# Kernel tuning notes

Measured on AMD Instinct MI355X. Metric: run time of the kernel, lower is better.

The kernel has to match this reference:

```python
import jax, jax.numpy as jnp
import numpy as np

B, S, D = 2, 2048, 4096
H, KVH, HD = 32, 8, 128
ROPE_THETA = 10000.0

def setup_inputs() -> dict:
    key = jax.random.key(0)
    ks = jax.random.split(key, 5)
    x = jax.random.normal(ks[0], (B, S, D), jnp.float32)
    wq = jax.random.normal(ks[1], (D, H * HD), jnp.float32) * 0.02
    wk = jax.random.normal(ks[2], (D, KVH * HD), jnp.float32) * 0.02
    wv = jax.random.normal(ks[3], (D, KVH * HD), jnp.float32) * 0.02
    wo = jax.random.normal(ks[4], (H * HD, D), jnp.float32) * 0.02
    pos = jnp.arange(S, dtype=jnp.float32)
    inv_freq = 1.0 / (ROPE_THETA ** (jnp.arange(0, HD, 2, dtype=jnp.float32) / HD))
    freqs = pos[:, None] * inv_freq[None, :]  # [S, HD//2]
    return {"x": x, "cos": jnp.cos(freqs), "sin": jnp.sin(freqs),
            "wq": wq, "wk": wk, "wv": wv, "wo": wo, "start_pos": 0}

def _apply_rope(t, cos, sin):
    # t: [B, S, nh, HD]; rotate consecutive pairs (llama complex rotation)
    t = t.reshape(*t.shape[:-1], HD // 2, 2)
    t1, t2 = t[..., 0], t[..., 1]
    c = cos[None, :, None, :]
    s = sin[None, :, None, :]
    out = jnp.stack([t1 * c - t2 * s, t1 * s + t2 * c], axis=-1)
    return out.reshape(*out.shape[:-2], HD)

def reference(x, cos, sin, wq, wk, wv, wo, start_pos):
    b, s, _ = x.shape
    scale = 1.0 / np.sqrt(HD)
    xq = (x @ wq).reshape(b, s, H, HD)
    xk = (x @ wk).reshape(b, s, KVH, HD)
    xv = (x @ wv).reshape(b, s, KVH, HD)
    xq = _apply_rope(xq, cos, sin)
    xk = _apply_rope(xk, cos, sin)
    # start_pos == 0 prefill: cache write then read of [:s] is identity
    n_rep = H // KVH
    keys = jnp.repeat(xk, n_rep, axis=2)    # [b, s, H, HD]
    values = jnp.repeat(xv, n_rep, axis=2)
    q = xq.transpose(0, 2, 1, 3)            # [b, H, s, HD]
    k = keys.transpose(0, 2, 1, 3)
    v = values.transpose(0, 2, 1, 3)
    scores = jnp.einsum('bhqd,bhkd->bhqk', q, k) * scale
    mask = jnp.triu(jnp.full((s, s), -jnp.inf, dtype=scores.dtype), k=1)
    scores = scores + mask[None, None]
    attn = jax.nn.softmax(scores.astype(jnp.float32), axis=-1).astype(q.dtype)
    out = jnp.einsum('bhqk,bhkd->bhqd', attn, v)
    out = out.transpose(0, 2, 1, 3).reshape(b, s, H * HD)
    return out @ wo
```

## Files before the change

kernel.cpp:

```cpp
#include <hip/hip_runtime.h>

typedef __bf16 bf16_t;
typedef __bf16 bf16x8 __attribute__((ext_vector_type(8)));
typedef __bf16 bf16x4 __attribute__((ext_vector_type(4)));
typedef float  f32x4  __attribute__((ext_vector_type(4)));
typedef float  f32x16 __attribute__((ext_vector_type(16)));

#define NB   2
#define NS   2048
#define ND   4096
#define NH   32
#define NKVH 8
#define NHD  128

#define BAR()     asm volatile("s_barrier" ::: "memory")
#define LGKM0()   asm volatile("s_waitcnt lgkmcnt(0)" ::: "memory")
#define VMCNT10() asm volatile("s_waitcnt vmcnt(10)" ::: "memory")
#define VMCNT8()  asm volatile("s_waitcnt vmcnt(8)" ::: "memory")
#define VMCNT6()  asm volatile("s_waitcnt vmcnt(6)" ::: "memory")
#define VMCNT0()  asm volatile("s_waitcnt vmcnt(0)" ::: "memory")

__device__ __forceinline__ void gl_lds16(const bf16_t* g, bf16_t* l) {
  __builtin_amdgcn_global_load_lds(
      (const __attribute__((address_space(1))) void*)g,
      (__attribute__((address_space(3))) void*)l, 16, 0, 0);
}

__global__ void convert_f32_bf16(const float* __restrict__ in, bf16_t* __restrict__ out, int n4) {
  int i = blockIdx.x * 256 + threadIdx.x;
  if (i < n4) {
    f32x4 v = *(const f32x4*)&in[(size_t)i * 4];
    bf16x4 o;
    #pragma unroll
    for (int j = 0; j < 4; ++j) o[j] = (bf16_t)v[j];
    *(bf16x4*)&out[(size_t)i * 4] = o;
  }
}

__global__ void transpose_convert(const float* __restrict__ in, bf16_t* __restrict__ out, int Nin) {
  __shared__ float t[32][33];
  int tx = threadIdx.x & 31, ty = threadIdx.x >> 5;
  int n0 = blockIdx.x * 32, k0 = blockIdx.y * 32;
  #pragma unroll
  for (int i = 0; i < 4; ++i)
    t[ty + i * 8][tx] = in[(size_t)(k0 + ty + i * 8) * Nin + n0 + tx];
  __syncthreads();
  #pragma unroll
  for (int i = 0; i < 4; ++i)
    out[(size_t)(n0 + ty + i * 8) * 4096 + k0 + tx] = (bf16_t)t[tx][ty + i * 8];
}

__global__ __launch_bounds__(256, 2) void gemm192(const bf16_t* __restrict__ A,
                                                  const bf16_t* __restrict__ Bt,
                                                  bf16_t* __restrict__ C, int M, int N, int K) {
  __shared__ __align__(16) bf16_t As[2][128 * 64];
  __shared__ __align__(16) bf16_t Bs[2][192 * 64];
  const int tid = threadIdx.x, lane = tid & 63, wid = tid >> 6;
  const int l15 = lane & 15, l4 = lane >> 4;
  const int wm = wid >> 1, wn = wid & 1;

  const int gx = gridDim.x;
  const int nwg = gx * gridDim.y;
  const int id = blockIdx.y * gx + blockIdx.x;
  const int wg = (id & 7) * (nwg >> 3) + (id >> 3);
  const int bx = wg % gx, by = wg / gx;
  const int row0 = bx * 128, col0 = by * 192;

  const bf16_t* Ab = A + (size_t)row0 * K;
  const bf16_t* Bb = Bt + (size_t)col0 * K;

  auto stA = [&](int t, int buf) {
    #pragma unroll
    for (int i = 0; i < 4; ++i) {
      int phys = i * 4096 + tid * 16;
      int logi = phys ^ (((phys >> 8) & 7) << 4);
      gl_lds16(Ab + (size_t)(logi >> 7) * K + t * 64 + ((logi & 127) >> 1),
               &As[buf][phys >> 1]);
    }
  };
  auto stB = [&](int t, int buf) {
    #pragma unroll
    for (int i = 0; i < 6; ++i) {
      int phys = i * 4096 + tid * 16;
      int logi = phys ^ (((phys >> 8) & 7) << 4);
      gl_lds16(Bb + (size_t)(logi >> 7) * K + t * 64 + ((logi & 127) >> 1),
               &Bs[buf][phys >> 1]);
    }
  };

  f32x4 acc[4][6];
  #pragma unroll
  for (int m = 0; m < 4; ++m)
    #pragma unroll
    for (int n = 0; n < 6; ++n)
      #pragma unroll
      for (int j = 0; j < 4; ++j) acc[m][n][j] = 0.f;

  const int nt = K >> 6;
  stA(0, 0); stB(0, 0);
  stA(1, 1); stB(1, 1);
  VMCNT10();
  BAR();

  auto ardA = [&](int buf, int mf, int kh) -> bf16x8 {
    int lb = (wm * 64 + mf * 16 + l15) * 128 + kh * 64 + l4 * 16;
    return *(const bf16x8*)&As[buf][(lb ^ (((lb >> 8) & 7) << 4)) >> 1];
  };
  auto brdB = [&](int buf, int kh, int nf) -> bf16x8 {
    int lb = (wn * 96 + nf * 16 + l15) * 128 + kh * 64 + l4 * 16;
    return *(const bf16x8*)&Bs[buf][(lb ^ (((lb >> 8) & 7) << 4)) >> 1];
  };

  #pragma unroll 2
  for (int t = 0; t < nt; ++t) {
    const int cur = t & 1;
    bf16x8 a[4][2], b0[6], b1[6];

    #pragma unroll
    for (int mf = 0; mf < 4; ++mf)
      #pragma unroll
      for (int kh = 0; kh < 2; ++kh) a[mf][kh] = ardA(cur, mf, kh);
    #pragma unroll
    for (int nf = 0; nf < 6; ++nf) b0[nf] = brdB(cur, 0, nf);
    BAR();
    LGKM0();
    __builtin_amdgcn_s_setprio(1);
    #pragma unroll
    for (int mf = 0; mf < 4; ++mf)
      #pragma unroll
      for (int nf = 0; nf < 6; ++nf)
        acc[mf][nf] = __builtin_amdgcn_mfma_f32_16x16x32_bf16(a[mf][0], b0[nf], acc[mf][nf], 0, 0, 0);
    __builtin_amdgcn_s_setprio(0);
    BAR();

    #pragma unroll
    for (int nf = 0; nf < 6; ++nf) b1[nf] = brdB(cur, 1, nf);
    if (t + 2 < nt) { stA(t + 2, cur); stB(t + 2, cur); }
    BAR();
    LGKM0();
    __builtin_amdgcn_s_setprio(1);
    #pragma unroll
    for (int mf = 0; mf < 4; ++mf)
      #pragma unroll
      for (int nf = 0; nf < 6; ++nf)
        acc[mf][nf] = __builtin_amdgcn_mfma_f32_16x16x32_bf16(a[mf][1], b1[nf], acc[mf][nf], 0, 0, 0);
    __builtin_amdgcn_s_setprio(0);
    if (t + 2 < nt) { VMCNT10(); } else { VMCNT0(); }
    BAR();
  }

  #pragma unroll
  for (int mf = 0; mf < 4; ++mf)
    #pragma unroll
    for (int nf = 0; nf < 6; ++nf)
      #pragma unroll
      for (int r = 0; r < 4; ++r) {
        size_t row = (size_t)row0 + wm * 64 + mf * 16 + l4 * 4 + r;
        size_t col = (size_t)col0 + wn * 96 + nf * 16 + l15;
        C[row * N + col] = (bf16_t)acc[mf][nf][r];
      }
}

__global__ __launch_bounds__(512, 2) void gemm256j(const bf16_t* __restrict__ A,
                                                   const bf16_t* __restrict__ Bt,
                                                   float* __restrict__ C, int M, int N, int K) {
  __shared__ __align__(16) bf16_t As[2][2][128 * 64];
  __shared__ __align__(16) bf16_t Bs[2][256 * 64];
  const int tid = threadIdx.x, lane = tid & 63, wid = tid >> 6;
  const int l15 = lane & 15, l4 = lane >> 4;
  const int wm = wid >> 2, wn = wid & 3;

  const int gx = gridDim.x;
  const int nwg = gx * gridDim.y;
  const int id = blockIdx.y * gx + blockIdx.x;
  const int wg = (id & 7) * (nwg >> 3) + (id >> 3);
  const int bx = wg % gx, by = wg / gx;
  const int row0 = bx * 256, col0 = by * 256;

  const bf16_t* Ab = A + (size_t)row0 * K;
  const bf16_t* Bb = Bt + (size_t)col0 * K;

  auto stA = [&](int t, int h, int buf) {
    #pragma unroll
    for (int i = 0; i < 2; ++i) {
      int phys = i * 8192 + tid * 16;
      int logi = phys ^ (((phys >> 8) & 7) << 4);
      gl_lds16(Ab + (size_t)(h * 128 + (logi >> 7)) * K + t * 64 + ((logi & 127) >> 1),
               &As[buf][h][phys >> 1]);
    }
  };
  auto stB = [&](int t, int buf) {
    #pragma unroll
    for (int i = 0; i < 4; ++i) {
      int phys = i * 8192 + tid * 16;
      int logi = phys ^ (((phys >> 8) & 7) << 4);
      gl_lds16(Bb + (size_t)(logi >> 7) * K + t * 64 + ((logi & 127) >> 1),
               &Bs[buf][phys >> 1]);
    }
  };

  f32x4 acc[8][4];
  #pragma unroll
  for (int m = 0; m < 8; ++m)
    #pragma unroll
    for (int n = 0; n < 4; ++n)
      #pragma unroll
      for (int j = 0; j < 4; ++j) acc[m][n][j] = 0.f;

  const int nt = K >> 6;
  stA(0, 0, 0); stA(0, 1, 0); stB(0, 0);
  stA(1, 0, 1); stB(1, 1);
  VMCNT6();
  BAR();

  auto ardA = [&](int buf, int mh, int kh, int mf) -> bf16x8 {
    int lb = (mh * 64 + mf * 16 + l15) * 128 + kh * 64 + l4 * 16;
    return *(const bf16x8*)&As[buf][wm][(lb ^ (((lb >> 8) & 7) << 4)) >> 1];
  };
  auto brdB = [&](int buf, int kh, int nf) -> bf16x8 {
    int lb = (wn * 64 + nf * 16 + l15) * 128 + kh * 64 + l4 * 16;
    return *(const bf16x8*)&Bs[buf][(lb ^ (((lb >> 8) & 7) << 4)) >> 1];
  };

  #pragma unroll 2
  for (int t = 0; t < nt; ++t) {
    const int cur = t & 1, nxt = cur ^ 1;
    bf16x8 a00[4], a01[4], a10[4], a11[4], b0[4], b1[4];

    #pragma unroll
    for (int mf = 0; mf < 4; ++mf) a00[mf] = ardA(cur, 0, 0, mf);
    #pragma unroll
    for (int nf = 0; nf < 4; ++nf) b0[nf] = brdB(cur, 0, nf);
    #pragma unroll
    for (int mf = 0; mf < 4; ++mf) a01[mf] = ardA(cur, 0, 1, mf);
    #pragma unroll
    for (int nf = 0; nf < 4; ++nf) b1[nf] = brdB(cur, 1, nf);
    if (t + 1 < nt) stA(t + 1, 1, nxt);
    BAR();
    LGKM0();
    __builtin_amdgcn_s_setprio(1);
    #pragma unroll
    for (int mf = 0; mf < 4; ++mf)
      #pragma unroll
      for (int nf = 0; nf < 4; ++nf)
        acc[mf][nf] = __builtin_amdgcn_mfma_f32_16x16x32_bf16(a00[mf], b0[nf], acc[mf][nf], 0, 0, 0);
    #pragma unroll
    for (int mf = 0; mf < 4; ++mf)
      #pragma unroll
      for (int nf = 0; nf < 4; ++nf)
        acc[mf][nf] = __builtin_amdgcn_mfma_f32_16x16x32_bf16(a01[mf], b1[nf], acc[mf][nf], 0, 0, 0);
    __builtin_amdgcn_s_setprio(0);
    BAR();

    #pragma unroll
    for (int mf = 0; mf < 4; ++mf) a10[mf] = ardA(cur, 1, 0, mf);
    #pragma unroll
    for (int mf = 0; mf < 4; ++mf) a11[mf] = ardA(cur, 1, 1, mf);
    if (t + 2 < nt) { stA(t + 2, 0, cur); stB(t + 2, cur); }
    BAR();
    LGKM0();
    __builtin_amdgcn_s_setprio(1);
    #pragma unroll
    for (int mf = 0; mf < 4; ++mf)
      #pragma unroll
      for (int nf = 0; nf < 4; ++nf)
        acc[4 + mf][nf] = __builtin_amdgcn_mfma_f32_16x16x32_bf16(a10[mf], b0[nf], acc[4 + mf][nf], 0, 0, 0);
    #pragma unroll
    for (int mf = 0; mf < 4; ++mf)
      #pragma unroll
      for (int nf = 0; nf < 4; ++nf)
        acc[4 + mf][nf] = __builtin_amdgcn_mfma_f32_16x16x32_bf16(a11[mf], b1[nf], acc[4 + mf][nf], 0, 0, 0);
    __builtin_amdgcn_s_setprio(0);
    if (t + 2 < nt) { VMCNT6(); } else { VMCNT0(); }
    BAR();
  }

  #pragma unroll
  for (int mh = 0; mh < 2; ++mh)
    #pragma unroll
    for (int mf = 0; mf < 4; ++mf)
      #pragma unroll
      for (int nf = 0; nf < 4; ++nf)
        #pragma unroll
        for (int r = 0; r < 4; ++r) {
          size_t row = (size_t)row0 + wm * 128 + mh * 64 + mf * 16 + l4 * 4 + r;
          size_t col = (size_t)col0 + wn * 64 + nf * 16 + l15;
          C[row * N + col] = acc[mh * 4 + mf][nf][r];
        }
}

__global__ void rope_qk(const bf16_t* __restrict__ qkv, const float* __restrict__ cosT,
                        const float* __restrict__ sinT, bf16_t* __restrict__ Q,
                        bf16_t* __restrict__ Kout) {
  int it = blockIdx.x * 256 + threadIdx.x;
  int chunk = it & 15;
  int hs = (it >> 4) % 40;
  int m = (it >> 4) / 40;
  int b = m >> 11, srow = m & 2047;

  bf16x8 v = *(const bf16x8*)&qkv[(size_t)m * 6144 + hs * 128 + chunk * 8];
  f32x4 c4 = *(const f32x4*)&cosT[(size_t)srow * 64 + chunk * 4];
  f32x4 s4 = *(const f32x4*)&sinT[(size_t)srow * 64 + chunk * 4];
  bf16x8 o;
  #pragma unroll
  for (int j = 0; j < 4; ++j) {
    float t1 = (float)v[2 * j], t2 = (float)v[2 * j + 1];
    o[2 * j]     = (bf16_t)(t1 * c4[j] - t2 * s4[j]);
    o[2 * j + 1] = (bf16_t)(t1 * s4[j] + t2 * c4[j]);
  }
  bf16_t* dst;
  if (hs < 32) dst = Q + (((size_t)(b * 32 + hs)) * 2048 + srow) * 128 + chunk * 8;
  else         dst = Kout + (((size_t)(b * 8 + (hs - 32))) * 2048 + srow) * 128 + chunk * 8;
  *(bf16x8*)dst = o;
}

__global__ void transpose_v(const bf16_t* __restrict__ qkv, bf16_t* __restrict__ Vt) {
  __shared__ bf16_t t[32][33];
  int tx = threadIdx.x & 31, ty = threadIdx.x >> 5;
  int s0 = blockIdx.x * 32, d0 = blockIdx.y * 32, g = blockIdx.z;
  int b = g >> 3, kv = g & 7;
  const bf16_t* src = qkv + (size_t)(b * 2048) * 6144 + 5120 + kv * 128;
  #pragma unroll
  for (int i = 0; i < 4; ++i)
    t[ty + i * 8][tx] = src[(size_t)(s0 + ty + i * 8) * 6144 + d0 + tx];
  __syncthreads();
  bf16_t* dst = Vt + (size_t)g * 128 * 2048;
  #pragma unroll
  for (int i = 0; i < 4; ++i)
    dst[(size_t)(d0 + ty + i * 8) * 2048 + s0 + tx] = t[tx][ty + i * 8];
}

__global__ __launch_bounds__(256, 2) void attn_kernel(const bf16_t* __restrict__ Q,
                                                      const bf16_t* __restrict__ Kc,
                                                      const bf16_t* __restrict__ Vt,
                                                      bf16_t* __restrict__ Oout) {
  __shared__ __align__(16) bf16_t Ks[2][64 * 128];
  __shared__ __align__(16) bf16_t Vs[2][128 * 64];

  const int tid = threadIdx.x, wid = tid >> 6, lane = tid & 63;
  const int l31 = lane & 31, hi = lane >> 5;
  const int bh = blockIdx.y;
  const int b = bh >> 5, h = bh & 31, kv = h >> 2;
  const int pr = blockIdx.x;

  const bf16_t* Qp = Q + ((size_t)bh * 2048) * 128;
  const bf16_t* Kp = Kc + ((size_t)(b * 8 + kv) * 2048) * 128;
  const bf16_t* Vp = Vt + ((size_t)(b * 8 + kv) * 128) * 2048;

  const float kscale = 0.08838834764831845f * 1.44269504088896f;

  auto stage = [&](int kt, int buf) {
    const int k0 = kt * 64;
    #pragma unroll
    for (int i = 0; i < 4; ++i) {
      int phys = i * 4096 + tid * 16;
      int logi = phys ^ (((phys >> 8) & 15) << 4);
      gl_lds16(Kp + (size_t)(k0 + (phys >> 8)) * 128 + ((logi & 255) >> 1), &Ks[buf][phys >> 1]);
    }
    #pragma unroll
    for (int i = 0; i < 4; ++i) {
      int phys = i * 4096 + tid * 16;
      int logi = phys ^ (((phys >> 7) & 7) << 4);
      gl_lds16(Vp + (size_t)(phys >> 7) * 2048 + k0 + ((logi & 127) >> 1), &Vs[buf][phys >> 1]);
    }
  };

  for (int half = 0; half < 2; ++half) {
    const int qt = half ? pr : 15 - pr;
    const int q0b = qt * 128;
    const int q0w = q0b + wid * 32;
    const int qg = q0w + l31;
    const int nkt = (qt + 1) * 2;

    bf16x8 qf[8];
    #pragma unroll
    for (int c = 0; c < 8; ++c) {
      bf16x8 t = *(const bf16x8*)&Qp[(size_t)qg * 128 + c * 16 + hi * 8];
      #pragma unroll
      for (int j = 0; j < 8; ++j) t[j] = (bf16_t)((float)t[j] * kscale);
      qf[c] = t;
    }

    f32x16 oa[4];
    #pragma unroll
    for (int nc = 0; nc < 4; ++nc)
      #pragma unroll
      for (int r = 0; r < 16; ++r) oa[nc][r] = 0.f;
    float m_old = -1e30f, lrow = 0.f;

    stage(0, 0);

    for (int kt = 0; kt < nkt; ++kt) {
      const int k0 = kt * 64, cur = kt & 1;
      if (kt + 1 < nkt) { stage(kt + 1, cur ^ 1); VMCNT8(); } else { VMCNT0(); }
      BAR();

      if (k0 <= q0w + 31) {
        f32x16 s0, s1;
        #pragma unroll
        for (int r = 0; r < 16; ++r) { s0[r] = 0.f; s1[r] = 0.f; }
        __builtin_amdgcn_s_setprio(1);
        #pragma unroll
        for (int c = 0; c < 8; ++c) {
          int lb0 = l31 * 256 + c * 32 + hi * 16;
          int pb0 = lb0 ^ (((lb0 >> 8) & 15) << 4);
          bf16x8 kf0 = *(const bf16x8*)&Ks[cur][pb0 >> 1];
          s0 = __builtin_amdgcn_mfma_f32_32x32x16_bf16(kf0, qf[c], s0, 0, 0, 0);
          int lb1 = (32 + l31) * 256 + c * 32 + hi * 16;
          int pb1 = lb1 ^ (((lb1 >> 8) & 15) << 4);
          bf16x8 kf1 = *(const bf16x8*)&Ks[cur][pb1 >> 1];
          s1 = __builtin_amdgcn_mfma_f32_32x32x16_bf16(kf1, qf[c], s1, 0, 0, 0);
        }
        __builtin_amdgcn_s_setprio(0);

        if (k0 + 63 > q0w) {
          #pragma unroll
          for (int r = 0; r < 16; ++r) {
            int key0 = k0 + ((r & 3) + 8 * (r >> 2)) + 4 * hi;
            if (key0 > qg) s0[r] = -1e30f;
            if (key0 + 32 > qg) s1[r] = -1e30f;
          }
        }

        float m8[8];
        #pragma unroll
        for (int j = 0; j < 8; ++j)
          m8[j] = fmaxf(fmaxf(s0[j], s0[j + 8]), fmaxf(s1[j], s1[j + 8]));
        float ma = fmaxf(fmaxf(m8[0], m8[4]), fmaxf(m8[1], m8[5]));
        float mb = fmaxf(fmaxf(m8[2], m8[6]), fmaxf(m8[3], m8[7]));
        float mh = fmaxf(ma, mb);
        float mfull = fmaxf(mh, __shfl_xor(mh, 32));

        float mn;
        bool defer = (mfull - m_old <= 8.0f);
        if (__all((int)defer)) {
          mn = m_old;
        } else {
          mn = fmaxf(m_old, mfull);
          float sc = exp2f(m_old - mn);
          #pragma unroll
          for (int r = 0; r < 16; ++r) {
            int qi = (r & 3) + 8 * (r >> 2) + 4 * hi;
            float scv = __int_as_float(__builtin_amdgcn_ds_bpermute(qi << 2, __float_as_int(sc)));
            oa[0][r] *= scv; oa[1][r] *= scv; oa[2][r] *= scv; oa[3][r] *= scv;
          }
          lrow *= sc;
          m_old = mn;
        }

        #pragma unroll
        for (int r = 0; r < 16; ++r) {
          s0[r] = exp2f(s0[r] - mn);
          s1[r] = exp2f(s1[r] - mn);
        }
        float rsA = 0.f, rsB = 0.f, rsC = 0.f, rsD = 0.f;
        #pragma unroll
        for (int r = 0; r < 16; r += 4) {
          rsA += s0[r];     rsB += s0[r + 1]; rsC += s0[r + 2]; rsD += s0[r + 3];
          rsA += s1[r];     rsB += s1[r + 1]; rsC += s1[r + 2]; rsD += s1[r + 3];
        }
        float rs = (rsA + rsB) + (rsC + rsD);
        rs += __shfl_xor(rs, 32);
        lrow = lrow + rs;

        #pragma unroll
        for (int ks = 0; ks < 4; ++ks) {
          const int qi0 = (ks & 1) * 8;
          union { bf16_t hh[4]; int ii[2]; } ku, su;
          #pragma unroll
          for (int j = 0; j < 4; ++j) {
            float lo, hv;
            if (ks >> 1) { lo = s1[qi0 + j]; hv = s1[qi0 + 4 + j]; }
            else         { lo = s0[qi0 + j]; hv = s0[qi0 + 4 + j]; }
            ku.hh[j] = (bf16_t)(hi ? hv : lo);
            su.hh[j] = (bf16_t)(hi ? lo : hv);
          }
          int r0 = __shfl_xor(su.ii[0], 32), r1 = __shfl_xor(su.ii[1], 32);
          union { int ii[4]; bf16x8 v; } fa;
          fa.ii[0] = hi ? r0 : ku.ii[0];
          fa.ii[1] = hi ? r1 : ku.ii[1];
          fa.ii[2] = hi ? ku.ii[0] : r0;
          fa.ii[3] = hi ? ku.ii[1] : r1;
          __builtin_amdgcn_s_setprio(1);
          #pragma unroll
          for (int nc = 0; nc < 4; ++nc) {
            int lb = (nc * 32 + l31) * 128 + ks * 32 + hi * 16;
            int pb = lb ^ (((lb >> 7) & 7) << 4);
            bf16x8 vf = *(const bf16x8*)&Vs[cur][pb >> 1];
            oa[nc] = __builtin_amdgcn_mfma_f32_32x32x16_bf16(fa.v, vf, oa[nc], 0, 0, 0);
          }
          __builtin_amdgcn_s_setprio(0);
        }
      }
      BAR();
    }

    float inv = 1.0f / lrow;
    bf16_t* Op = Oout + ((size_t)(b * 2048 + q0w)) * 4096 + (size_t)h * 128;
    #pragma unroll
    for (int r = 0; r < 16; ++r) {
      int qi = (r & 3) + 8 * (r >> 2) + 4 * hi;
      float iv = __int_as_float(__builtin_amdgcn_ds_bpermute(qi << 2, __float_as_int(inv)));
      #pragma unroll
      for (int nc = 0; nc < 4; ++nc)
        Op[(size_t)qi * 4096 + nc * 32 + l31] = (bf16_t)(oa[nc][r] * iv);
    }
  }
}

extern "C" void kernel_launch(void* const* d_in, const int* in_sizes, int n_in,
                              void* d_out, int out_size, void* d_ws, size_t ws_size,
                              hipStream_t stream) {
  const float* x    = (const float*)d_in[0];
  const float* cosT = (const float*)d_in[1];
  const float* sinT = (const float*)d_in[2];
  const float* wq   = (const float*)d_in[3];
  const float* wk   = (const float*)d_in[4];
  const float* wv   = (const float*)d_in[5];
  const float* wo   = (const float*)d_in[6];
  float* out = (float*)d_out;
  char* ws = (char*)d_ws;

  bf16_t* wqkvT = (bf16_t*)(ws + 0);
  bf16_t* woT   = wqkvT;
  bf16_t* xb    = (bf16_t*)(ws + 50331648);
  bf16_t* Qb    = xb;
  bf16_t* qkv   = (bf16_t*)(ws + 83886080);
  bf16_t* attn_out = qkv;
  bf16_t* Kb    = (bf16_t*)(ws + 134217728);
  bf16_t* Vt    = (bf16_t*)(ws + 142606336);

  convert_f32_bf16<<<16384, 256, 0, stream>>>(x, xb, 4194304);
  transpose_convert<<<dim3(128, 128), 256, 0, stream>>>(wq, wqkvT, 4096);
  transpose_convert<<<dim3(32, 128), 256, 0, stream>>>(wk, wqkvT + (size_t)4096 * 4096, 1024);
  transpose_convert<<<dim3(32, 128), 256, 0, stream>>>(wv, wqkvT + (size_t)5120 * 4096, 1024);

  gemm192<<<dim3(32, 32), 256, 0, stream>>>(xb, wqkvT, qkv, 4096, 6144, 4096);

  transpose_convert<<<dim3(128, 128), 256, 0, stream>>>(wo, woT, 4096);
  rope_qk<<<10240, 256, 0, stream>>>(qkv, cosT, sinT, Qb, Kb);
  transpose_v<<<dim3(64, 4, 16), 256, 0, stream>>>(qkv, Vt);

  attn_kernel<<<dim3(8, 64), 256, 0, stream>>>(Qb, Kb, Vt, attn_out);

  gemm256j<<<dim3(16, 16), 512, 0, stream>>>(attn_out, woT, out, 4096, 4096, 4096);
}
```

Before: 512.4 us.

## Replace 256x256 output-projection GEMM with 128x128 tile kernel

The output projection GEMM moves from a 512-thread kernel with 256x256 tiles and a split A-stage pipeline to a 256-thread kernel with 128x128 tiles and a simpler double-buffered pipeline. The grid grows from 256 to 1024 workgroups, which gives better coverage of the MI355X's many CUs and smaller LDS and register footprints per block. In exchange, arithmetic intensity per tile is lower, so more global and LDS traffic is spent per FLOP. The pipeline stages are rearranged, with B's second K-half loaded in the middle phase.

```diff
diff --git a/kernel.cpp b/kernel.cpp
--- a/kernel.cpp
+++ b/kernel.cpp
@@ -17,7 +17,6 @@
 #define LGKM0()   asm volatile("s_waitcnt lgkmcnt(0)" ::: "memory")
 #define VMCNT10() asm volatile("s_waitcnt vmcnt(10)" ::: "memory")
 #define VMCNT8()  asm volatile("s_waitcnt vmcnt(8)" ::: "memory")
-#define VMCNT6()  asm volatile("s_waitcnt vmcnt(6)" ::: "memory")
 #define VMCNT0()  asm volatile("s_waitcnt vmcnt(0)" ::: "memory")
 
 __device__ __forceinline__ void gl_lds16(const bf16_t* g, bf16_t* l) {
@@ -161,61 +160,61 @@
       }
 }
 
-__global__ __launch_bounds__(512, 2) void gemm256j(const bf16_t* __restrict__ A,
-                                                   const bf16_t* __restrict__ Bt,
-                                                   float* __restrict__ C, int M, int N, int K) {
-  __shared__ __align__(16) bf16_t As[2][2][128 * 64];
-  __shared__ __align__(16) bf16_t Bs[2][256 * 64];
+__global__ __launch_bounds__(256, 2) void gemm128(const bf16_t* __restrict__ A,
+                                                  const bf16_t* __restrict__ Bt,
+                                                  float* __restrict__ C, int M, int N, int K) {
+  __shared__ __align__(16) bf16_t As[2][128 * 64];
+  __shared__ __align__(16) bf16_t Bs[2][128 * 64];
   const int tid = threadIdx.x, lane = tid & 63, wid = tid >> 6;
   const int l15 = lane & 15, l4 = lane >> 4;
-  const int wm = wid >> 2, wn = wid & 3;
+  const int wm = wid >> 1, wn = wid & 1;
 
   const int gx = gridDim.x;
   const int nwg = gx * gridDim.y;
   const int id = blockIdx.y * gx + blockIdx.x;
   const int wg = (id & 7) * (nwg >> 3) + (id >> 3);
   const int bx = wg % gx, by = wg / gx;
-  const int row0 = bx * 256, col0 = by * 256;
+  const int row0 = bx * 128, col0 = by * 128;
 
   const bf16_t* Ab = A + (size_t)row0 * K;
   const bf16_t* Bb = Bt + (size_t)col0 * K;
 
-  auto stA = [&](int t, int h, int buf) {
-    #pragma unroll
-    for (int i = 0; i < 2; ++i) {
-      int phys = i * 8192 + tid * 16;
+  auto stA = [&](int t, int buf) {
+    #pragma unroll
+    for (int i = 0; i < 4; ++i) {
+      int phys = i * 4096 + tid * 16;
       int logi = phys ^ (((phys >> 8) & 7) << 4);
-      gl_lds16(Ab + (size_t)(h * 128 + (logi >> 7)) * K + t * 64 + ((logi & 127) >> 1),
-               &As[buf][h][phys >> 1]);
+      gl_lds16(Ab + (size_t)(logi >> 7) * K + t * 64 + ((logi & 127) >> 1),
+               &As[buf][phys >> 1]);
     }
   };
   auto stB = [&](int t, int buf) {
     #pragma unroll
     for (int i = 0; i < 4; ++i) {
-      int phys = i * 8192 + tid * 16;
+      int phys = i * 4096 + tid * 16;
       int logi = phys ^ (((phys >> 8) & 7) << 4);
       gl_lds16(Bb + (size_t)(logi >> 7) * K + t * 64 + ((logi & 127) >> 1),
                &Bs[buf][phys >> 1]);
     }
   };
 
-  f32x4 acc[8][4];
-  #pragma unroll
-  for (int m = 0; m < 8; ++m)
+  f32x4 acc[4][4];
+  #pragma unroll
+  for (int m = 0; m < 4; ++m)
     #pragma unroll
     for (int n = 0; n < 4; ++n)
       #pragma unroll
       for (int j = 0; j < 4; ++j) acc[m][n][j] = 0.f;
 
   const int nt = K >> 6;
-  stA(0, 0, 0); stA(0, 1, 0); stB(0, 0);
-  stA(1, 0, 1); stB(1, 1);
-  VMCNT6();
+  stA(0, 0); stB(0, 0);
+  stA(1, 1); stB(1, 1);
+  VMCNT8();
   BAR();
 
-  auto ardA = [&](int buf, int mh, int kh, int mf) -> bf16x8 {
-    int lb = (mh * 64 + mf * 16 + l15) * 128 + kh * 64 + l4 * 16;
-    return *(const bf16x8*)&As[buf][wm][(lb ^ (((lb >> 8) & 7) << 4)) >> 1];
+  auto ardA = [&](int buf, int mf, int kh) -> bf16x8 {
+    int lb = (wm * 64 + mf * 16 + l15) * 128 + kh * 64 + l4 * 16;
+    return *(const bf16x8*)&As[buf][(lb ^ (((lb >> 8) & 7) << 4)) >> 1];
   };
   auto brdB = [&](int buf, int kh, int nf) -> bf16x8 {
     int lb = (wn * 64 + nf * 16 + l15) * 128 + kh * 64 + l4 * 16;
@@ -224,18 +223,15 @@
 
   #pragma unroll 2
   for (int t = 0; t < nt; ++t) {
-    const int cur = t & 1, nxt = cur ^ 1;
-    bf16x8 a00[4], a01[4], a10[4], a11[4], b0[4], b1[4];
-
-    #pragma unroll
-    for (int mf = 0; mf < 4; ++mf) a00[mf] = ardA(cur, 0, 0, mf);
+    const int cur = t & 1;
+    bf16x8 a[4][2], b0[4], b1[4];
+
+    #pragma unroll
+    for (int mf = 0; mf < 4; ++mf)
+      #pragma unroll
+      for (int kh = 0; kh < 2; ++kh) a[mf][kh] = ardA(cur, mf, kh);
     #pragma unroll
     for (int nf = 0; nf < 4; ++nf) b0[nf] = brdB(cur, 0, nf);
-    #pragma unroll
-    for (int mf = 0; mf < 4; ++mf) a01[mf] = ardA(cur, 0, 1, mf);
-    #pragma unroll
-    for (int nf = 0; nf < 4; ++nf) b1[nf] = brdB(cur, 1, nf);
-    if (t + 1 < nt) stA(t + 1, 1, nxt);
     BAR();
     LGKM0();
     __builtin_amdgcn_s_setprio(1);
@@ -243,20 +239,13 @@
     for (int mf = 0; mf < 4; ++mf)
       #pragma unroll
       for (int nf = 0; nf < 4; ++nf)
-        acc[mf][nf] = __builtin_amdgcn_mfma_f32_16x16x32_bf16(a00[mf], b0[nf], acc[mf][nf], 0, 0, 0);
-    #pragma unroll
-    for (int mf = 0; mf < 4; ++mf)
-      #pragma unroll
-      for (int nf = 0; nf < 4; ++nf)
-        acc[mf][nf] = __builtin_amdgcn_mfma_f32_16x16x32_bf16(a01[mf], b1[nf], acc[mf][nf], 0, 0, 0);
+        acc[mf][nf] = __builtin_amdgcn_mfma_f32_16x16x32_bf16(a[mf][0], b0[nf], acc[mf][nf], 0, 0, 0);
     __builtin_amdgcn_s_setprio(0);
     BAR();
 
     #pragma unroll
-    for (int mf = 0; mf < 4; ++mf) a10[mf] = ardA(cur, 1, 0, mf);
-    #pragma unroll
-    for (int mf = 0; mf < 4; ++mf) a11[mf] = ardA(cur, 1, 1, mf);
-    if (t + 2 < nt) { stA(t + 2, 0, cur); stB(t + 2, cur); }
+    for (int nf = 0; nf < 4; ++nf) b1[nf] = brdB(cur, 1, nf);
+    if (t + 2 < nt) { stA(t + 2, cur); stB(t + 2, cur); }
     BAR();
     LGKM0();
     __builtin_amdgcn_s_setprio(1);
@@ -264,29 +253,22 @@
     for (int mf = 0; mf < 4; ++mf)
       #pragma unroll
       for (int nf = 0; nf < 4; ++nf)
-        acc[4 + mf][nf] = __builtin_amdgcn_mfma_f32_16x16x32_bf16(a10[mf], b0[nf], acc[4 + mf][nf], 0, 0, 0);
-    #pragma unroll
-    for (int mf = 0; mf < 4; ++mf)
-      #pragma unroll
-      for (int nf = 0; nf < 4; ++nf)
-        acc[4 + mf][nf] = __builtin_amdgcn_mfma_f32_16x16x32_bf16(a11[mf], b1[nf], acc[4 + mf][nf], 0, 0, 0);
+        acc[mf][nf] = __builtin_amdgcn_mfma_f32_16x16x32_bf16(a[mf][1], b1[nf], acc[mf][nf], 0, 0, 0);
     __builtin_amdgcn_s_setprio(0);
-    if (t + 2 < nt) { VMCNT6(); } else { VMCNT0(); }
+    if (t + 2 < nt) { VMCNT8(); } else { VMCNT0(); }
     BAR();
   }
 
   #pragma unroll
-  for (int mh = 0; mh < 2; ++mh)
-    #pragma unroll
-    for (int mf = 0; mf < 4; ++mf)
-      #pragma unroll
-      for (int nf = 0; nf < 4; ++nf)
-        #pragma unroll
-        for (int r = 0; r < 4; ++r) {
-          size_t row = (size_t)row0 + wm * 128 + mh * 64 + mf * 16 + l4 * 4 + r;
-          size_t col = (size_t)col0 + wn * 64 + nf * 16 + l15;
-          C[row * N + col] = acc[mh * 4 + mf][nf][r];
-        }
+  for (int mf = 0; mf < 4; ++mf)
+    #pragma unroll
+    for (int nf = 0; nf < 4; ++nf)
+      #pragma unroll
+      for (int r = 0; r < 4; ++r) {
+        size_t row = (size_t)row0 + wm * 64 + mf * 16 + l4 * 4 + r;
+        size_t col = (size_t)col0 + wn * 64 + nf * 16 + l15;
+        C[row * N + col] = acc[mf][nf][r];
+      }
 }
 
 __global__ void rope_qk(const bf16_t* __restrict__ qkv, const float* __restrict__ cosT,
@@ -543,5 +525,5 @@
 
   attn_kernel<<<dim3(8, 64), 256, 0, stream>>>(Qb, Kb, Vt, attn_out);
 
-  gemm256j<<<dim3(16, 16), 512, 0, stream>>>(attn_out, woT, out, 4096, 4096, 4096);
-}
+  gemm128<<<dim3(32, 32), 256, 0, stream>>>(attn_out, woT, out, 4096, 4096, 4096);
+}
```

New measurement: 526.5 us. 2.7% more time.
